# Kernel tuning notes

Hardware: AMD Instinct MI355X
Metric: run time of the kernel (lower is better)

The kernel has to match this reference:

```python
import jax, jax.numpy as jnp
import numpy as np

N_NODES = 100000
N_EDGES = 1600000
HIDDEN = 128
N_LAYERS = 4
EPS = 0.0  # GINConv default eps, train_eps=False


def setup_inputs() -> dict:
    key = jax.random.key(0)
    ks = jax.random.split(key, 6)
    scale = 1.0 / np.sqrt(HIDDEN)
    return {
        "x": jax.random.normal(ks[0], (N_NODES, HIDDEN), dtype=jnp.float32),
        "edge_index": jax.random.randint(ks[1], (2, N_EDGES), 0, N_NODES, dtype=jnp.int64),
        "W1": jax.random.normal(ks[2], (N_LAYERS, HIDDEN, HIDDEN), dtype=jnp.float32) * scale,
        "b1": jnp.zeros((N_LAYERS, HIDDEN), dtype=jnp.float32),
        "W2": jax.random.normal(ks[3], (N_LAYERS, HIDDEN, HIDDEN), dtype=jnp.float32) * scale,
        "b2": jnp.zeros((N_LAYERS, HIDDEN), dtype=jnp.float32),
    }


def reference(x, edge_index, W1, b1, W2, b2):
    src = edge_index[0]  # message sources (x_j)
    dst = edge_index[1]  # aggregation targets
    n = x.shape[0]
    for l in range(N_LAYERS):
        x_in = x
        # scatter-add aggregation: sum_{j in N(i)} x_j
        agg = jax.ops.segment_sum(x[src], dst, num_segments=n)
        out = agg + (1.0 + EPS) * x
        # GIN MLP: Linear -> ReLU -> Linear
        h = jax.nn.relu(out @ W1[l] + b1[l]) @ W2[l] + b2[l]
        # outer loop: relu, dropout (identity in eval), residual
        x = x_in + jax.nn.relu(h)
    return x
```

## Files before the change

kernel.cpp:

```cpp
#include <hip/hip_runtime.h>

typedef unsigned short u16;
typedef unsigned int u32;
typedef unsigned char u8;

constexpr int NN = 100000;
constexpr int NE = 1600000;
constexpr int H = 128;

constexpr int NB = 196;
constexpr int BCAP = 10240;
constexpr int PB_E = 4096;
constexpr int PB_BLOCKS = (NE + PB_E - 1) / PB_E;
constexpr int WT_BLOCKS = 512;
constexpr int XI_BLOCKS = (NN * H / 4) / 256;

typedef __bf16 bf16x8 __attribute__((ext_vector_type(8)));
typedef float f32x16 __attribute__((ext_vector_type(16)));

__device__ __forceinline__ u16 f2bf(float f) {
    union { float f; u32 u; } cv; cv.f = f;
    u32 r = (cv.u + 0x7fffu + ((cv.u >> 16) & 1u)) >> 16;
    return (u16)r;
}
__device__ __forceinline__ float bflo(u32 u) {
    union { u32 u; float f; } cv; cv.u = u << 16; return cv.f;
}
__device__ __forceinline__ float bfhi(u32 u) {
    union { u32 u; float f; } cv; cv.u = u & 0xffff0000u; return cv.f;
}
__device__ __forceinline__ u32 pkbf(float a, float b) {
    return (u32)f2bf(a) | ((u32)f2bf(b) << 16);
}

__global__ __launch_bounds__(256) void preproc_kernel(const int* __restrict__ e,
                                                      int* __restrict__ gcursor,
                                                      u32* __restrict__ ebuf,
                                                      const float* __restrict__ W1,
                                                      const float* __restrict__ W2,
                                                      u16* __restrict__ wt,
                                                      const float* __restrict__ xin,
                                                      float* __restrict__ x,
                                                      u16* __restrict__ xb) {
    __shared__ int lcnt[256];
    __shared__ int ps[256];
    __shared__ int ex[256];
    __shared__ int gbaseL[NB];
    __shared__ int anynz;
    __shared__ u32 sbuf[PB_E];
    __shared__ u8 sbk[PB_E];
    const int blk = blockIdx.x;
    const int t = threadIdx.x;

    if (blk >= PB_BLOCKS) {
        if (blk < PB_BLOCKS + WT_BLOCKS) {
            int tt = (blk - PB_BLOCKS) * 256 + t;
            int w = tt >> 14;
            int r = tt & 16383;
            int k = r >> 7, n = r & 127;
            int l = w >> 1, s = w & 1;
            const float* src = (s == 0 ? W1 : W2) + l * 16384;
            wt[w * 16384 + n * 128 + k] = f2bf(src[k * 128 + n]);
        } else {
            int i = (blk - PB_BLOCKS - WT_BLOCKS) * 256 + t;
            float4 v = ((const float4*)xin)[i];
            ((float4*)x)[i] = v;
            uint2 p;
            p.x = pkbf(v.x, v.y);
            p.y = pkbf(v.z, v.w);
            ((uint2*)xb)[i] = p;
        }
        return;
    }

    if (t == 0) anynz = 0;
    lcnt[t] = 0;
    __syncthreads();
    int loc = 0;
    for (int i = t; i < 4096; i += 256) loc |= e[2 * i + 1];
    if (loc) atomicOr(&anynz, 1);
    __syncthreads();
    const int st = anynz ? 1 : 2;
    const int base = blk * PB_E;
    const int nval = (NE - base < PB_E) ? (NE - base) : PB_E;
    u32 pk[16]; int bk[16]; int rk[16];
#pragma unroll
    for (int j = 0; j < 16; ++j) {
        int i = base + j * 256 + t;
        bk[j] = -1;
        if (i < NE) {
            int s = e[st * i];
            int d = e[st * (NE + i)];
            int b = d >> 9;
            pk[j] = (u32)s | ((u32)(d & 511) << 17);
            bk[j] = b;
            rk[j] = atomicAdd(&lcnt[b], 1);
        }
    }
    __syncthreads();
    int v = lcnt[t];
    ps[t] = v;
    __syncthreads();
    for (int off = 1; off < 256; off <<= 1) {
        int u = (t >= off) ? ps[t - off] : 0;
        __syncthreads();
        ps[t] += u;
        __syncthreads();
    }
    ex[t] = ps[t] - v;
    if (t < NB && v > 0) gbaseL[t] = atomicAdd(&gcursor[t], v);
    __syncthreads();
#pragma unroll
    for (int j = 0; j < 16; ++j)
        if (bk[j] >= 0) {
            int p = ex[bk[j]] + rk[j];
            sbuf[p] = pk[j];
            sbk[p] = (u8)bk[j];
        }
    __syncthreads();
    for (int i = t; i < nval; i += 256) {
        int b = sbk[i];
        ebuf[b * BCAP + gbaseL[b] + (i - ex[b])] = sbuf[i];
    }
}

__global__ __launch_bounds__(256) void bfill_kernel(const u32* __restrict__ ebuf,
                                                    const int* __restrict__ gcursor,
                                                    int* __restrict__ offs,
                                                    int* __restrict__ colv) {
    __shared__ int ncnt[512];
    __shared__ int cur[512];
    __shared__ int ps[256];
    const int b = blockIdx.x, t = threadIdx.x;
    const int En = gcursor[b];
    int gv = (t < NB) ? gcursor[t] : 0;
    ps[t] = gv;
    __syncthreads();
    for (int off = 1; off < 256; off <<= 1) {
        int u = (t >= off) ? ps[t - off] : 0;
        __syncthreads();
        ps[t] += u;
        __syncthreads();
    }
    const int bb = ps[b] - En;
    if (b == 0 && t == 0) offs[NN] = NE;
    ncnt[t] = 0; ncnt[t + 256] = 0;
    __syncthreads();
    const u32* eb = ebuf + b * BCAP;
    for (int i = t; i < En; i += 256)
        atomicAdd(&ncnt[eb[i] >> 17], 1);
    __syncthreads();
    int s2 = ncnt[2 * t] + ncnt[2 * t + 1];
    ps[t] = s2;
    __syncthreads();
    for (int off = 1; off < 256; off <<= 1) {
        int u = (t >= off) ? ps[t - off] : 0;
        __syncthreads();
        ps[t] += u;
        __syncthreads();
    }
    int e0 = ps[t] - s2;
    cur[2 * t] = e0;
    cur[2 * t + 1] = e0 + ncnt[2 * t];
    __syncthreads();
    const int n0 = b * 512;
    for (int i = t; i < 512; i += 256)
        if (n0 + i < NN) offs[n0 + i] = bb + cur[i];
    __syncthreads();
    for (int i = t; i < En; i += 256) {
        u32 p = eb[i];
        int pos = atomicAdd(&cur[p >> 17], 1);
        colv[bb + pos] = (int)((p & 0x1FFFFu) | (((p >> 17) & 31u) << 27));
    }
}

__global__ __launch_bounds__(256) void mlp_kernel(const u16* __restrict__ xbin,
                                                  const int* __restrict__ colv,
                                                  const int* __restrict__ offs,
                                                  const u16* __restrict__ wt1,
                                                  const u16* __restrict__ wt2,
                                                  const float* __restrict__ b1,
                                                  const float* __restrict__ b2,
                                                  float* __restrict__ x,
                                                  u16* __restrict__ xbout) {
    __shared__ u16 lds[32 * 128];
    const int tid = threadIdx.x;
    const int wave = tid >> 6, lane = tid & 63;
    const int ml = lane & 31, g = lane >> 5;
    const int row0 = blockIdx.x * 32;

#pragma unroll
    for (int i = 0; i < 2; ++i) {
        int ch = tid + 256 * i;
        int r = ch >> 4, c = ch & 15;
        int gr = row0 + r;
        int4 v = *(const int4*)(xbin + gr * H + c * 8);
        *(int4*)(&lds[r * H + ((c ^ (r & 15)) << 3)]) = v;
    }
    __syncthreads();

    {
        const int node0 = row0 + wave * 8;
        const int jb = __builtin_amdgcn_readfirstlane(offs[node0]);
        const int je = __builtin_amdgcn_readfirstlane(offs[node0 + 8]);
        int cur = wave * 8;
        float a0 = 0.f, a1 = 0.f;
        if (jb < je) {
            u32 ce[16];
#pragma unroll
            for (int q = 0; q < 16; ++q) {
                int idx = jb + q;
                idx = idx < je ? idx : je - 1;
                ce[q] = (u32)__builtin_amdgcn_readfirstlane(colv[idx]);
            }
            for (int j = jb; j < je; j += 16) {
                u32 uu[16];
#pragma unroll
                for (int q = 0; q < 16; ++q)
                    uu[q] = *(const u32*)(xbin + (ce[q] & 0x1FFFFu) * H + lane * 2);
                u32 cn[16];
#pragma unroll
                for (int q = 0; q < 16; ++q) {
                    int idx = j + 16 + q;
                    idx = idx < je ? idx : je - 1;
                    cn[q] = (u32)__builtin_amdgcn_readfirstlane(colv[idx]);
                }
#pragma unroll
                for (int q = 0; q < 16; ++q) {
                    if (j + q < je) {
                        int rloc = (int)(ce[q] >> 27);
                        if (rloc != cur) {
                            u16* p = &lds[cur * H + (((lane >> 2) ^ (cur & 15)) << 3) + ((lane & 3) << 1)];
                            u32 old = *(u32*)p;
                            *(u32*)p = pkbf(bflo(old) + a0, bfhi(old) + a1);
                            a0 = 0.f; a1 = 0.f; cur = rloc;
                        }
                        a0 += bflo(uu[q]); a1 += bfhi(uu[q]);
                    }
                }
#pragma unroll
                for (int q = 0; q < 16; ++q) ce[q] = cn[q];
            }
        }
        u16* p = &lds[cur * H + (((lane >> 2) ^ (cur & 15)) << 3) + ((lane & 3) << 1)];
        u32 old = *(u32*)p;
        *(u32*)p = pkbf(bflo(old) + a0, bfhi(old) + a1);
    }

    bf16x8 bfrag[8];
#pragma unroll
    for (int ks = 0; ks < 8; ++ks)
        bfrag[ks] = *(const bf16x8*)(wt1 + (wave * 32 + ml) * H + ks * 16 + g * 8);
    const float bias1 = b1[wave * 32 + ml];
    const float bias2 = b2[wave * 32 + ml];

    __syncthreads();

    f32x16 acc;
#pragma unroll
    for (int i = 0; i < 16; ++i) acc[i] = 0.f;

#pragma unroll
    for (int ks = 0; ks < 8; ++ks) {
        int chunk = (2 * ks + g) ^ (ml & 15);
        bf16x8 afrag = *(const bf16x8*)(&lds[ml * H + (chunk << 3)]);
        acc = __builtin_amdgcn_mfma_f32_32x32x16_bf16(afrag, bfrag[ks], acc, 0, 0, 0);
    }

    __syncthreads();

#pragma unroll
    for (int reg = 0; reg < 16; ++reg) {
        int rm = (reg & 3) + ((reg >> 2) << 3) + 4 * g;
        int cn = wave * 32 + ml;
        float v = acc[reg] + bias1;
        v = v > 0.f ? v : 0.f;
        lds[rm * H + ((((cn >> 3) ^ (rm & 15))) << 3) + (cn & 7)] = f2bf(v);
    }

#pragma unroll
    for (int ks = 0; ks < 8; ++ks)
        bfrag[ks] = *(const bf16x8*)(wt2 + (wave * 32 + ml) * H + ks * 16 + g * 8);

#pragma unroll
    for (int i = 0; i < 16; ++i) acc[i] = 0.f;

    __syncthreads();

#pragma unroll
    for (int ks = 0; ks < 8; ++ks) {
        int chunk = (2 * ks + g) ^ (ml & 15);
        bf16x8 afrag = *(const bf16x8*)(&lds[ml * H + (chunk << 3)]);
        acc = __builtin_amdgcn_mfma_f32_32x32x16_bf16(afrag, bfrag[ks], acc, 0, 0, 0);
    }

    __syncthreads();

#pragma unroll
    for (int reg = 0; reg < 16; ++reg) {
        int rm = (reg & 3) + ((reg >> 2) << 3) + 4 * g;
        int cn = wave * 32 + ml;
        float v = acc[reg] + bias2;
        v = v > 0.f ? v : 0.f;
        lds[rm * H + ((((cn >> 3) ^ (rm & 15))) << 3) + (cn & 7)] = f2bf(v);
    }

    __syncthreads();

#pragma unroll
    for (int i = 0; i < 2; ++i) {
        int ch = tid + 256 * i;
        int r = ch >> 4, c = ch & 15;
        int gr = row0 + r;
        int4 hv = *(const int4*)(&lds[r * H + ((c ^ (r & 15)) << 3)]);
        float4 x0 = *(const float4*)(x + gr * H + c * 8);
        float4 x1 = *(const float4*)(x + gr * H + c * 8 + 4);
        x0.x += bflo((u32)hv.x); x0.y += bfhi((u32)hv.x);
        x0.z += bflo((u32)hv.y); x0.w += bfhi((u32)hv.y);
        x1.x += bflo((u32)hv.z); x1.y += bfhi((u32)hv.z);
        x1.z += bflo((u32)hv.w); x1.w += bfhi((u32)hv.w);
        *(float4*)(x + gr * H + c * 8) = x0;
        *(float4*)(x + gr * H + c * 8 + 4) = x1;
        int4 xo;
        xo.x = (int)pkbf(x0.x, x0.y);
        xo.y = (int)pkbf(x0.z, x0.w);
        xo.z = (int)pkbf(x1.x, x1.y);
        xo.w = (int)pkbf(x1.z, x1.w);
        *(int4*)(xbout + gr * H + c * 8) = xo;
    }
}

extern "C" void kernel_launch(void* const* d_in, const int* in_sizes, int n_in,
                              void* d_out, int out_size, void* d_ws, size_t ws_size,
                              hipStream_t stream) {
    const float* x_in = (const float*)d_in[0];
    const int* edges = (const int*)d_in[1];
    const float* W1 = (const float*)d_in[2];
    const float* b1 = (const float*)d_in[3];
    const float* W2 = (const float*)d_in[4];
    const float* b2 = (const float*)d_in[5];
    float* x = (float*)d_out;

    char* ws = (char*)d_ws;
    int* gcursor = (int*)(ws + 512);
    int* offs = (int*)(ws + 4096);
    int* colv = (int*)(ws + 406528);
    u16* wt = (u16*)(ws + 6809600);
    u16* xb0 = (u16*)(ws + 7072768);
    u16* xb1 = (u16*)(ws + 32672768);
    u32* ebuf = (u32*)xb1;

    hipMemsetAsync(gcursor, 0, NB * sizeof(int), stream);
    preproc_kernel<<<PB_BLOCKS + WT_BLOCKS + XI_BLOCKS, 256, 0, stream>>>(
        edges, gcursor, ebuf, W1, W2, wt, x_in, x, xb0);
    bfill_kernel<<<NB, 256, 0, stream>>>(ebuf, gcursor, offs, colv);

    for (int l = 0; l < 4; ++l) {
        u16* xin = (l & 1) ? xb1 : xb0;
        u16* xout = (l & 1) ? xb0 : xb1;
        mlp_kernel<<<NN / 32, 256, 0, stream>>>(
            xin, colv, offs,
            wt + (l * 2) * 16384, wt + (l * 2 + 1) * 16384,
            b1 + l * 128, b2 + l * 128, x, xout);
    }
}
```

Baseline: 474.2 us.

## Split aggregation into column-sliced gather kernel with sliced bf16 feature layout

Pulls the neighbor aggregation out of the fused MLP kernel into a separate agg_kernel. The bf16 node features are stored as 8 column slices of 16 features each, and each block gathers a single slice, so one slice's working set (about 3.2 MB) is more likely to stay in cache during the random gathers. The MLP kernel now reads the precomputed aggregate, which already includes the self term, and writes its output in the sliced layout. The cost is an extra kernel launch per layer and an extra global round trip for the aggregate buffer.

```diff
diff --git a/kernel.cpp b/kernel.cpp
--- a/kernel.cpp
+++ b/kernel.cpp
@@ -41,7 +41,7 @@
                                                       u16* __restrict__ wt,
                                                       const float* __restrict__ xin,
                                                       float* __restrict__ x,
-                                                      u16* __restrict__ xb) {
+                                                      u16* __restrict__ xbs) {
     __shared__ int lcnt[256];
     __shared__ int ps[256];
     __shared__ int ex[256];
@@ -65,10 +65,10 @@
             int i = (blk - PB_BLOCKS - WT_BLOCKS) * 256 + t;
             float4 v = ((const float4*)xin)[i];
             ((float4*)x)[i] = v;
-            uint2 p;
-            p.x = pkbf(v.x, v.y);
-            p.y = pkbf(v.z, v.w);
-            ((uint2*)xb)[i] = p;
+            int n = i >> 5;
+            int j = i & 31;
+            u32* dst = (u32*)xbs + (size_t)(j >> 2) * (NN * 8) + n * 8 + (j & 3) * 2;
+            ((uint2*)dst)[0] = make_uint2(pkbf(v.x, v.y), pkbf(v.z, v.w));
         }
         return;
     }
@@ -170,19 +170,53 @@
     for (int i = t; i < En; i += 256) {
         u32 p = eb[i];
         int pos = atomicAdd(&cur[p >> 17], 1);
-        colv[bb + pos] = (int)((p & 0x1FFFFu) | (((p >> 17) & 31u) << 27));
-    }
-}
-
-__global__ __launch_bounds__(256) void mlp_kernel(const u16* __restrict__ xbin,
+        colv[bb + pos] = (int)(p & 0x1FFFFu);
+    }
+}
+
+__global__ __launch_bounds__(256) void agg_kernel(const u16* __restrict__ xbsin,
                                                   const int* __restrict__ colv,
                                                   const int* __restrict__ offs,
+                                                  u16* __restrict__ aggb) {
+    const int cg = blockIdx.x & 7;
+    const int tile = blockIdx.x >> 3;
+    const int lane = threadIdx.x & 63;
+    const int wave = threadIdx.x >> 6;
+    const int o = lane >> 3, cl = lane & 7;
+    const int n = tile * 32 + wave * 8 + o;
+    const u32* slice = (const u32*)xbsin + (size_t)cg * (NN * 8);
+    const int jb = offs[n];
+    const int je = offs[n + 1];
+    u32 sv = slice[n * 8 + cl];
+    float a0 = bflo(sv), a1 = bfhi(sv);
+    for (int j = jb; j < je; j += 8) {
+        int src[8]; u32 mk[8];
+#pragma unroll
+        for (int q = 0; q < 8; ++q) {
+            int idx = j + q < je ? j + q : je - 1;
+            mk[q] = (j + q < je) ? 0xffffffffu : 0u;
+            src[q] = __builtin_nontemporal_load(colv + idx) & 0x1FFFF;
+        }
+        u32 vv[8];
+#pragma unroll
+        for (int q = 0; q < 8; ++q) vv[q] = slice[src[q] * 8 + cl];
+#pragma unroll
+        for (int q = 0; q < 8; ++q) {
+            u32 u = vv[q] & mk[q];
+            a0 += bflo(u); a1 += bfhi(u);
+        }
+    }
+    __builtin_nontemporal_store(pkbf(a0, a1),
+                                (u32*)aggb + (size_t)cg * (NN * 8) + n * 8 + cl);
+}
+
+__global__ __launch_bounds__(256) void mlp_kernel(const u16* __restrict__ aggb,
                                                   const u16* __restrict__ wt1,
                                                   const u16* __restrict__ wt2,
                                                   const float* __restrict__ b1,
                                                   const float* __restrict__ b2,
                                                   float* __restrict__ x,
-                                                  u16* __restrict__ xbout) {
+                                                  u16* __restrict__ xbsout) {
     __shared__ u16 lds[32 * 128];
     const int tid = threadIdx.x;
     const int wave = tid >> 6, lane = tid & 63;
@@ -193,58 +227,9 @@
     for (int i = 0; i < 2; ++i) {
         int ch = tid + 256 * i;
         int r = ch >> 4, c = ch & 15;
-        int gr = row0 + r;
-        int4 v = *(const int4*)(xbin + gr * H + c * 8);
+        const u16* src = aggb + (size_t)(c >> 1) * (NN * 16) + (row0 + r) * 16 + (c & 1) * 8;
+        int4 v = *(const int4*)src;
         *(int4*)(&lds[r * H + ((c ^ (r & 15)) << 3)]) = v;
-    }
-    __syncthreads();
-
-    {
-        const int node0 = row0 + wave * 8;
-        const int jb = __builtin_amdgcn_readfirstlane(offs[node0]);
-        const int je = __builtin_amdgcn_readfirstlane(offs[node0 + 8]);
-        int cur = wave * 8;
-        float a0 = 0.f, a1 = 0.f;
-        if (jb < je) {
-            u32 ce[16];
-#pragma unroll
-            for (int q = 0; q < 16; ++q) {
-                int idx = jb + q;
-                idx = idx < je ? idx : je - 1;
-                ce[q] = (u32)__builtin_amdgcn_readfirstlane(colv[idx]);
-            }
-            for (int j = jb; j < je; j += 16) {
-                u32 uu[16];
-#pragma unroll
-                for (int q = 0; q < 16; ++q)
-                    uu[q] = *(const u32*)(xbin + (ce[q] & 0x1FFFFu) * H + lane * 2);
-                u32 cn[16];
-#pragma unroll
-                for (int q = 0; q < 16; ++q) {
-                    int idx = j + 16 + q;
-                    idx = idx < je ? idx : je - 1;
-                    cn[q] = (u32)__builtin_amdgcn_readfirstlane(colv[idx]);
-                }
-#pragma unroll
-                for (int q = 0; q < 16; ++q) {
-                    if (j + q < je) {
-                        int rloc = (int)(ce[q] >> 27);
-                        if (rloc != cur) {
-                            u16* p = &lds[cur * H + (((lane >> 2) ^ (cur & 15)) << 3) + ((lane & 3) << 1)];
-                            u32 old = *(u32*)p;
-                            *(u32*)p = pkbf(bflo(old) + a0, bfhi(old) + a1);
-                            a0 = 0.f; a1 = 0.f; cur = rloc;
-                        }
-                        a0 += bflo(uu[q]); a1 += bfhi(uu[q]);
-                    }
-                }
-#pragma unroll
-                for (int q = 0; q < 16; ++q) ce[q] = cn[q];
-            }
-        }
-        u16* p = &lds[cur * H + (((lane >> 2) ^ (cur & 15)) << 3) + ((lane & 3) << 1)];
-        u32 old = *(u32*)p;
-        *(u32*)p = pkbf(bflo(old) + a0, bfhi(old) + a1);
     }
 
     bf16x8 bfrag[8];
@@ -326,7 +311,7 @@
         xo.y = (int)pkbf(x0.z, x0.w);
         xo.z = (int)pkbf(x1.x, x1.y);
         xo.w = (int)pkbf(x1.z, x1.w);
-        *(int4*)(xbout + gr * H + c * 8) = xo;
+        *(int4*)(xbsout + (size_t)(c >> 1) * (NN * 16) + gr * 16 + (c & 1) * 8) = xo;
     }
 }
 
@@ -346,21 +331,22 @@
     int* offs = (int*)(ws + 4096);
     int* colv = (int*)(ws + 406528);
     u16* wt = (u16*)(ws + 6809600);
-    u16* xb0 = (u16*)(ws + 7072768);
-    u16* xb1 = (u16*)(ws + 32672768);
-    u32* ebuf = (u32*)xb1;
+    u16* xbs0 = (u16*)(ws + 7072768);
+    u16* xbs1 = (u16*)(ws + 32672768);
+    u16* aggb = (u16*)(ws + 58272768);
+    u32* ebuf = (u32*)aggb;
 
     hipMemsetAsync(gcursor, 0, NB * sizeof(int), stream);
     preproc_kernel<<<PB_BLOCKS + WT_BLOCKS + XI_BLOCKS, 256, 0, stream>>>(
-        edges, gcursor, ebuf, W1, W2, wt, x_in, x, xb0);
+        edges, gcursor, ebuf, W1, W2, wt, x_in, x, xbs0);
     bfill_kernel<<<NB, 256, 0, stream>>>(ebuf, gcursor, offs, colv);
 
     for (int l = 0; l < 4; ++l) {
-        u16* xin = (l & 1) ? xb1 : xb0;
-        u16* xout = (l & 1) ? xb0 : xb1;
+        u16* xin = (l & 1) ? xbs1 : xbs0;
+        u16* xout = (l & 1) ? xbs0 : xbs1;
+        agg_kernel<<<(NN / 32) * 8, 256, 0, stream>>>(xin, colv, offs, aggb);
         mlp_kernel<<<NN / 32, 256, 0, stream>>>(
-            xin, colv, offs,
-            wt + (l * 2) * 16384, wt + (l * 2 + 1) * 16384,
+            aggb, wt + (l * 2) * 16384, wt + (l * 2 + 1) * 16384,
             b1 + l * 128, b2 + l * 128, x, xout);
     }
 }
```

After: 933.9 us. 1.97x slower.
